# Kernel optimization log

Hardware: AMD Instinct MI355X
Metric: run time of the kernel (lower is better)

The kernel has to match this reference:

```python
import jax, jax.numpy as jnp
import numpy as np

B, N, D_IN, D_OUT = 16, 4096, 256, 128


def setup_inputs() -> dict:
    key = jax.random.key(0)
    ks = jax.random.split(key, 7)
    s_proj = float(np.sqrt(2.0 / D_IN))   # kaiming-ish scale
    s_mlp = float(np.sqrt(2.0 / D_OUT))
    return {
        "X": jax.random.normal(ks[0], (B, N, D_IN), dtype=jnp.float32),
        "W_proj": jax.random.normal(ks[1], (D_IN, D_OUT), dtype=jnp.float32) * s_proj,
        "b_proj": jnp.zeros((D_OUT,), dtype=jnp.float32),
        "W1": jax.random.normal(ks[2], (D_OUT, D_OUT), dtype=jnp.float32) * s_mlp,
        "b1": jnp.zeros((D_OUT,), dtype=jnp.float32),
        "W2": jax.random.normal(ks[3], (D_OUT, D_OUT), dtype=jnp.float32) * s_mlp,
        "b2": jnp.zeros((D_OUT,), dtype=jnp.float32),
    }


def reference(X, W_proj, b_proj, W1, b1, W2, b2):
    # proj: Linear(input_dim, output_dim)
    X = jnp.einsum("bnd,de->bne", X, W_proj) + b_proj
    # mlp: FeedForwardNetwork(D,D,D, num_layers=2) == Linear -> ReLU -> Linear
    X = jax.nn.relu(jnp.einsum("bnd,de->bne", X, W1) + b1)
    X = jnp.einsum("bnd,de->bne", X, W2) + b2
    # leave-one-out sum over the N axis: for each row i, sum of all rows j != i.
    # Identical math to the masked (B,N,N,D) expand-reduce in the torch source.
    return X.sum(axis=1, keepdims=True) - X
```

## Files before the change

kernel.cpp:

```cpp
#include <hip/hip_runtime.h>
#include <stdint.h>

#define D_IN  256
#define D_OUT 128
#define NSEQ  4096
#define NB    16
#define TILE_M 64
#define GRID_M ((NB * NSEQ) / TILE_M)
#define LDS_BYTES 32768

typedef __bf16 bf16x8 __attribute__((ext_vector_type(8)));
typedef float  f32x4  __attribute__((ext_vector_type(4)));

__device__ __forceinline__ unsigned short f2bf(float f) {
  __bf16 h = (__bf16)f;
  union { __bf16 h; unsigned short u; } c; c.h = h;
  return c.u;
}
__device__ __forceinline__ float bf2f(unsigned short u) {
  union { unsigned int u; float f; } a; a.u = ((unsigned int)u) << 16;
  return a.f;
}

__global__ __launch_bounds__(256) void prep(
    const float* __restrict__ Wp, const float* __restrict__ W1, const float* __restrict__ W2,
    const float* __restrict__ bp, const float* __restrict__ b1,
    unsigned short* __restrict__ WaT, unsigned short* __restrict__ W2T, float* __restrict__ be1) {
  int b = blockIdx.x;
  if (b < 128) {
    __shared__ float wp[256];
    int k0 = b * 2;
    wp[threadIdx.x] = Wp[k0 * 128 + threadIdx.x];
    __syncthreads();
    int kk = threadIdx.x >> 7, n = threadIdx.x & 127;
    float s = 0.f;
#pragma unroll 16
    for (int j = 0; j < 128; ++j) s += wp[kk * 128 + j] * W1[j * 128 + n];
    WaT[n * 256 + (k0 + kk)] = f2bf(s);
  } else if (b < 192) {
    int t = (b - 128) * 256 + threadIdx.x;
    int k = t >> 7, n = t & 127;
    W2T[n * 128 + k] = f2bf(W2[t]);
  } else {
    if (threadIdx.x < 128) {
      int n = threadIdx.x;
      float s = b1[n];
#pragma unroll 16
      for (int j = 0; j < 128; ++j) s += bp[j] * W1[j * 128 + n];
      be1[n] = s;
    }
  }
}

template <bool USE_WS>
__global__ __launch_bounds__(256, 3) void fused2(
    const float* __restrict__ X,
    const unsigned short* __restrict__ WaT,
    const unsigned short* __restrict__ W2T,
    const float* __restrict__ be1, const float* __restrict__ b2v,
    unsigned short* __restrict__ Y3, float* __restrict__ out, float* __restrict__ P) {
  extern __shared__ unsigned short smem[];
  unsigned short* bufA = smem;
  unsigned short* bufB = smem + 8192;

  const int tid  = threadIdx.x;
  const int lane = tid & 63;
  const int w    = tid >> 6;
  const int q    = lane >> 4;
  const int l16  = lane & 15;
  const int rowbase = blockIdx.x * TILE_M;
  const int col0 = w * 32 + l16;
  const int col1 = col0 + 16;

  f32x4 acc[4][2];
  bf16x8 bA[4][2], bB[4][2];

#pragma unroll
  for (int ks = 0; ks < 4; ++ks) {
    bA[ks][0] = *(const bf16x8*)(WaT + (size_t)col0 * 256 + ks * 32 + q * 8);
    bA[ks][1] = *(const bf16x8*)(WaT + (size_t)col1 * 256 + ks * 32 + q * 8);
  }

#pragma unroll
  for (int it = 0; it < 8; ++it) {
    int i = tid + it * 256;
    int r = i >> 5, c4 = (i & 31) << 2;
    const float4 v = *(const float4*)(X + (size_t)(rowbase + r) * D_IN + c4);
    ushort4 u; u.x = f2bf(v.x); u.y = f2bf(v.y); u.z = f2bf(v.z); u.w = f2bf(v.w);
    *(ushort4*)(bufA + r * 128 + ((((c4 >> 3) ^ (r & 15)) << 3) + (c4 & 7))) = u;
  }

#pragma unroll
  for (int rt = 0; rt < 4; ++rt) {
    acc[rt][0] = (f32x4){0.f, 0.f, 0.f, 0.f};
    acc[rt][1] = (f32x4){0.f, 0.f, 0.f, 0.f};
  }
  __syncthreads();

  float4 xv[8];
#pragma unroll
  for (int it = 0; it < 8; ++it) {
    int i = tid + it * 256;
    int r = i >> 5, c4 = (i & 31) << 2;
    xv[it] = *(const float4*)(X + (size_t)(rowbase + r) * D_IN + 128 + c4);
  }
#pragma unroll
  for (int ks = 0; ks < 4; ++ks) {
    bB[ks][0] = *(const bf16x8*)(WaT + (size_t)col0 * 256 + 128 + ks * 32 + q * 8);
    bB[ks][1] = *(const bf16x8*)(WaT + (size_t)col1 * 256 + 128 + ks * 32 + q * 8);
  }

#pragma unroll
  for (int ks = 0; ks < 4; ++ks)
#pragma unroll
    for (int rt = 0; rt < 4; ++rt) {
      bf16x8 a = *(const bf16x8*)(bufA + (rt * 16 + l16) * 128 + (((4 * ks + q) ^ l16) << 3));
      acc[rt][0] = __builtin_amdgcn_mfma_f32_16x16x32_bf16(a, bA[ks][0], acc[rt][0], 0, 0, 0);
      acc[rt][1] = __builtin_amdgcn_mfma_f32_16x16x32_bf16(a, bA[ks][1], acc[rt][1], 0, 0, 0);
    }

#pragma unroll
  for (int it = 0; it < 8; ++it) {
    int i = tid + it * 256;
    int r = i >> 5, c4 = (i & 31) << 2;
    ushort4 u; u.x = f2bf(xv[it].x); u.y = f2bf(xv[it].y); u.z = f2bf(xv[it].z); u.w = f2bf(xv[it].w);
    *(ushort4*)(bufB + r * 128 + ((((c4 >> 3) ^ (r & 15)) << 3) + (c4 & 7))) = u;
  }
  __syncthreads();

#pragma unroll
  for (int ks = 0; ks < 4; ++ks) {
    bA[ks][0] = *(const bf16x8*)(W2T + (size_t)col0 * 128 + ks * 32 + q * 8);
    bA[ks][1] = *(const bf16x8*)(W2T + (size_t)col1 * 128 + ks * 32 + q * 8);
  }

#pragma unroll
  for (int ks = 0; ks < 4; ++ks)
#pragma unroll
    for (int rt = 0; rt < 4; ++rt) {
      bf16x8 a = *(const bf16x8*)(bufB + (rt * 16 + l16) * 128 + (((4 * ks + q) ^ l16) << 3));
      acc[rt][0] = __builtin_amdgcn_mfma_f32_16x16x32_bf16(a, bB[ks][0], acc[rt][0], 0, 0, 0);
      acc[rt][1] = __builtin_amdgcn_mfma_f32_16x16x32_bf16(a, bB[ks][1], acc[rt][1], 0, 0, 0);
    }

  {
    const float e0 = be1[col0], e1 = be1[col1];
#pragma unroll
    for (int rt = 0; rt < 4; ++rt)
#pragma unroll
      for (int r = 0; r < 4; ++r) {
        int row = rt * 16 + q * 4 + r;
        int sw = (row & 15) << 3;
        float v0 = acc[rt][0][r] + e0; v0 = v0 > 0.f ? v0 : 0.f;
        float v1 = acc[rt][1][r] + e1; v1 = v1 > 0.f ? v1 : 0.f;
        bufA[row * 128 + ((((col0 >> 3) << 3) ^ sw) + (col0 & 7))] = f2bf(v0);
        bufA[row * 128 + ((((col1 >> 3) << 3) ^ sw) + (col1 & 7))] = f2bf(v1);
      }
  }
  __syncthreads();

#pragma unroll
  for (int rt = 0; rt < 4; ++rt) {
    acc[rt][0] = (f32x4){0.f, 0.f, 0.f, 0.f};
    acc[rt][1] = (f32x4){0.f, 0.f, 0.f, 0.f};
  }
#pragma unroll
  for (int ks = 0; ks < 4; ++ks)
#pragma unroll
    for (int rt = 0; rt < 4; ++rt) {
      bf16x8 a = *(const bf16x8*)(bufA + (rt * 16 + l16) * 128 + (((4 * ks + q) ^ l16) << 3));
      acc[rt][0] = __builtin_amdgcn_mfma_f32_16x16x32_bf16(a, bA[ks][0], acc[rt][0], 0, 0, 0);
      acc[rt][1] = __builtin_amdgcn_mfma_f32_16x16x32_bf16(a, bA[ks][1], acc[rt][1], 0, 0, 0);
    }

  {
    const float bb0 = b2v[col0], bb1 = b2v[col1];
    float s0 = 0.f, s1 = 0.f;
#pragma unroll
    for (int rt = 0; rt < 4; ++rt)
#pragma unroll
      for (int r = 0; r < 4; ++r) {
        int row = rt * 16 + q * 4 + r;
        int sw = (row & 15) << 3;
        float v0 = acc[rt][0][r] + bb0;
        float v1 = acc[rt][1][r] + bb1;
        s0 += v0; s1 += v1;
        bufB[row * 128 + ((((col0 >> 3) << 3) ^ sw) + (col0 & 7))] = f2bf(v0);
        bufB[row * 128 + ((((col1 >> 3) << 3) ^ sw) + (col1 & 7))] = f2bf(v1);
      }
    s0 += __shfl_down(s0, 16); s0 += __shfl_down(s0, 32);
    s1 += __shfl_down(s1, 16); s1 += __shfl_down(s1, 32);
    if (lane < 16) {
      P[(size_t)blockIdx.x * 128 + col0] = s0;
      P[(size_t)blockIdx.x * 128 + col1] = s1;
    }
  }
  __syncthreads();

  if (USE_WS) {
#pragma unroll
    for (int it = 0; it < 4; ++it) {
      int i = tid + it * 256;
      int r = i >> 4, g = i & 15;
      *(uint4*)(Y3 + (size_t)(rowbase + r) * 128 + g * 8) =
          *(const uint4*)(bufB + r * 128 + ((g ^ (r & 15)) << 3));
    }
  } else {
#pragma unroll
    for (int it = 0; it < 8; ++it) {
      int i = tid + it * 256;
      int r = i >> 5, c4 = (i & 31) << 2;
      ushort4 u = *(const ushort4*)(bufB + r * 128 + ((((c4 >> 3) ^ (r & 15)) << 3) + (c4 & 7)));
      float4 v; v.x = bf2f(u.x); v.y = bf2f(u.y); v.z = bf2f(u.z); v.w = bf2f(u.w);
      *(float4*)(out + (size_t)(rowbase + r) * D_OUT + c4) = v;
    }
  }
}

__global__ __launch_bounds__(256) void reduce_S(const float* __restrict__ P, float* __restrict__ S) {
  __shared__ float tmp[128];
  int b = blockIdx.x;
  int col = threadIdx.x & 127;
  int h = threadIdx.x >> 7;
  float s = 0.f;
#pragma unroll
  for (int i = 0; i < 32; ++i) s += P[(size_t)(b * 64 + h * 32 + i) * 128 + col];
  if (h == 1) tmp[col] = s;
  __syncthreads();
  if (h == 0) S[b * 128 + col] = s + tmp[col];
}

__global__ __launch_bounds__(256) void finalize_ws(
    float* __restrict__ out, const unsigned short* __restrict__ Y3, const float* __restrict__ S) {
  size_t g = (size_t)blockIdx.x * 256 + threadIdx.x;
  size_t base = g * 8;
  int row = (int)(base >> 7);
  int col = (int)(base & 127);
  int b = row >> 12;
  uint4 u = *(const uint4*)(Y3 + base);
  float4 s0 = *(const float4*)(S + (b << 7) + col);
  float4 s1 = *(const float4*)(S + (b << 7) + col + 4);
  union { unsigned int uu; float f; } t;
  float4 o0, o1;
  t.uu = u.x << 16;          o0.x = s0.x - t.f;
  t.uu = u.x & 0xFFFF0000u;  o0.y = s0.y - t.f;
  t.uu = u.y << 16;          o0.z = s0.z - t.f;
  t.uu = u.y & 0xFFFF0000u;  o0.w = s0.w - t.f;
  t.uu = u.z << 16;          o1.x = s1.x - t.f;
  t.uu = u.z & 0xFFFF0000u;  o1.y = s1.y - t.f;
  t.uu = u.w << 16;          o1.z = s1.z - t.f;
  t.uu = u.w & 0xFFFF0000u;  o1.w = s1.w - t.f;
  *(float4*)(out + base) = o0;
  *(float4*)(out + base + 4) = o1;
}

__global__ __launch_bounds__(256) void finalize_ip(float* __restrict__ out, const float* __restrict__ S) {
  size_t g = (size_t)blockIdx.x * 256 + threadIdx.x;
  size_t base = g * 8;
  int row = (int)(base >> 7);
  int col = (int)(base & 127);
  int b = row >> 12;
  float4 s0 = *(const float4*)(S + (b << 7) + col);
  float4 s1 = *(const float4*)(S + (b << 7) + col + 4);
  float4 y0 = *(const float4*)(out + base);
  float4 y1 = *(const float4*)(out + base + 4);
  float4 o0, o1;
  o0.x = s0.x - y0.x; o0.y = s0.y - y0.y; o0.z = s0.z - y0.z; o0.w = s0.w - y0.w;
  o1.x = s1.x - y1.x; o1.y = s1.y - y1.y; o1.z = s1.z - y1.z; o1.w = s1.w - y1.w;
  *(float4*)(out + base) = o0;
  *(float4*)(out + base + 4) = o1;
}

extern "C" void kernel_launch(void* const* d_in, const int* in_sizes, int n_in,
                              void* d_out, int out_size, void* d_ws, size_t ws_size,
                              hipStream_t stream) {
  const float* X  = (const float*)d_in[0];
  const float* Wp = (const float*)d_in[1];
  const float* bp = (const float*)d_in[2];
  const float* W1 = (const float*)d_in[3];
  const float* b1 = (const float*)d_in[4];
  const float* W2 = (const float*)d_in[5];
  const float* b2 = (const float*)d_in[6];
  float* out = (float*)d_out;

  char* ws = (char*)d_ws;
  float* S            = (float*)ws;
  float* be1          = (float*)(ws + 8192);
  unsigned short* WaT = (unsigned short*)(ws + 12288);
  unsigned short* W2T = (unsigned short*)(ws + 12288 + 65536);
  float* P            = (float*)(ws + 12288 + 65536 + 32768);
  unsigned short* Y3  = (unsigned short*)(ws + 12288 + 65536 + 32768 + 524288);

  const size_t need = 12288 + 65536 + 32768 + 524288 + (size_t)NB * NSEQ * D_OUT * 2;
  const bool use_ws = ws_size >= need;

  prep<<<193, 256, 0, stream>>>(Wp, W1, W2, bp, b1, WaT, W2T, be1);

  const int fin_blocks = (NB * NSEQ * D_OUT) / (8 * 256);
  if (use_ws) {
    fused2<true><<<GRID_M, 256, LDS_BYTES, stream>>>(X, WaT, W2T, be1, b2, Y3, out, P);
    reduce_S<<<NB, 256, 0, stream>>>(P, S);
    finalize_ws<<<fin_blocks, 256, 0, stream>>>(out, Y3, S);
  } else {
    fused2<false><<<GRID_M, 256, LDS_BYTES, stream>>>(X, WaT, W2T, be1, b2, Y3, out, P);
    reduce_S<<<NB, 256, 0, stream>>>(P, S);
    finalize_ip<<<fin_blocks, 256, 0, stream>>>(out, S);
  }
}
```

Baseline: 134.0 us.

## Fuse per-batch column reduction into GEMM kernel via last-block atomic counter

Removes the separate reduce_S launch: each block bumps a per-batch atomic counter after writing its partial sums, and the last of the 64 blocks for a batch reduces the partials into S. The counters are zeroed in the prep kernel. X loading is also restructured so all 256 input columns are loaded up front into registers (16 float4 per thread) and written to both LDS halves before the first GEMM, rather than overlapping the second-half load with the first MFMA pass. This saves one kernel launch and gap, at the cost of more register pressure, fences, and lost overlap of the second X load.

```diff
diff --git a/kernel.cpp b/kernel.cpp
--- a/kernel.cpp
+++ b/kernel.cpp
@@ -25,7 +25,8 @@
 __global__ __launch_bounds__(256) void prep(
     const float* __restrict__ Wp, const float* __restrict__ W1, const float* __restrict__ W2,
     const float* __restrict__ bp, const float* __restrict__ b1,
-    unsigned short* __restrict__ WaT, unsigned short* __restrict__ W2T, float* __restrict__ be1) {
+    unsigned short* __restrict__ WaT, unsigned short* __restrict__ W2T,
+    float* __restrict__ be1, int* __restrict__ cnt) {
   int b = blockIdx.x;
   if (b < 128) {
     __shared__ float wp[256];
@@ -49,6 +50,7 @@
       for (int j = 0; j < 128; ++j) s += bp[j] * W1[j * 128 + n];
       be1[n] = s;
     }
+    if (threadIdx.x < NB) cnt[threadIdx.x] = 0;
   }
 }
 
@@ -58,10 +60,13 @@
     const unsigned short* __restrict__ WaT,
     const unsigned short* __restrict__ W2T,
     const float* __restrict__ be1, const float* __restrict__ b2v,
-    unsigned short* __restrict__ Y3, float* __restrict__ out, float* __restrict__ P) {
+    unsigned short* __restrict__ Y3, float* __restrict__ out,
+    float* __restrict__ P, float* __restrict__ S, int* __restrict__ cnt) {
   extern __shared__ unsigned short smem[];
   unsigned short* bufA = smem;
   unsigned short* bufB = smem + 8192;
+  __shared__ float red[128];
+  __shared__ int isLast;
 
   const int tid  = threadIdx.x;
   const int lane = tid & 63;
@@ -69,46 +74,44 @@
   const int q    = lane >> 4;
   const int l16  = lane & 15;
   const int rowbase = blockIdx.x * TILE_M;
+  const int bidx = blockIdx.x >> 6;
   const int col0 = w * 32 + l16;
   const int col1 = col0 + 16;
 
-  f32x4 acc[4][2];
+  float4 xv[16];
+#pragma unroll
+  for (int it = 0; it < 16; ++it) {
+    int i = tid + it * 256;
+    int r = i >> 6, c4 = (i & 63) << 2;
+    xv[it] = *(const float4*)(X + (size_t)(rowbase + r) * D_IN + c4);
+  }
+#pragma unroll
+  for (int it = 0; it < 16; ++it) {
+    int i = tid + it * 256;
+    int r = i >> 6, c4 = (i & 63) << 2;
+    unsigned short* dst = (c4 < 128) ? bufA : bufB;
+    int cc = c4 & 127;
+    ushort4 u; u.x = f2bf(xv[it].x); u.y = f2bf(xv[it].y); u.z = f2bf(xv[it].z); u.w = f2bf(xv[it].w);
+    *(ushort4*)(dst + r * 128 + ((((cc >> 3) ^ (r & 15)) << 3) + (cc & 7))) = u;
+  }
+
   bf16x8 bA[4][2], bB[4][2];
-
 #pragma unroll
   for (int ks = 0; ks < 4; ++ks) {
     bA[ks][0] = *(const bf16x8*)(WaT + (size_t)col0 * 256 + ks * 32 + q * 8);
     bA[ks][1] = *(const bf16x8*)(WaT + (size_t)col1 * 256 + ks * 32 + q * 8);
-  }
-
-#pragma unroll
-  for (int it = 0; it < 8; ++it) {
-    int i = tid + it * 256;
-    int r = i >> 5, c4 = (i & 31) << 2;
-    const float4 v = *(const float4*)(X + (size_t)(rowbase + r) * D_IN + c4);
-    ushort4 u; u.x = f2bf(v.x); u.y = f2bf(v.y); u.z = f2bf(v.z); u.w = f2bf(v.w);
-    *(ushort4*)(bufA + r * 128 + ((((c4 >> 3) ^ (r & 15)) << 3) + (c4 & 7))) = u;
-  }
-
+    bB[ks][0] = *(const bf16x8*)(WaT + (size_t)col0 * 256 + 128 + ks * 32 + q * 8);
+    bB[ks][1] = *(const bf16x8*)(WaT + (size_t)col1 * 256 + 128 + ks * 32 + q * 8);
+  }
+  __builtin_amdgcn_sched_barrier(0);
+
+  f32x4 acc[4][2];
 #pragma unroll
   for (int rt = 0; rt < 4; ++rt) {
     acc[rt][0] = (f32x4){0.f, 0.f, 0.f, 0.f};
     acc[rt][1] = (f32x4){0.f, 0.f, 0.f, 0.f};
   }
   __syncthreads();
-
-  float4 xv[8];
-#pragma unroll
-  for (int it = 0; it < 8; ++it) {
-    int i = tid + it * 256;
-    int r = i >> 5, c4 = (i & 31) << 2;
-    xv[it] = *(const float4*)(X + (size_t)(rowbase + r) * D_IN + 128 + c4);
-  }
-#pragma unroll
-  for (int ks = 0; ks < 4; ++ks) {
-    bB[ks][0] = *(const bf16x8*)(WaT + (size_t)col0 * 256 + 128 + ks * 32 + q * 8);
-    bB[ks][1] = *(const bf16x8*)(WaT + (size_t)col1 * 256 + 128 + ks * 32 + q * 8);
-  }
 
 #pragma unroll
   for (int ks = 0; ks < 4; ++ks)
@@ -118,22 +121,6 @@
       acc[rt][0] = __builtin_amdgcn_mfma_f32_16x16x32_bf16(a, bA[ks][0], acc[rt][0], 0, 0, 0);
       acc[rt][1] = __builtin_amdgcn_mfma_f32_16x16x32_bf16(a, bA[ks][1], acc[rt][1], 0, 0, 0);
     }
-
-#pragma unroll
-  for (int it = 0; it < 8; ++it) {
-    int i = tid + it * 256;
-    int r = i >> 5, c4 = (i & 31) << 2;
-    ushort4 u; u.x = f2bf(xv[it].x); u.y = f2bf(xv[it].y); u.z = f2bf(xv[it].z); u.w = f2bf(xv[it].w);
-    *(ushort4*)(bufB + r * 128 + ((((c4 >> 3) ^ (r & 15)) << 3) + (c4 & 7))) = u;
-  }
-  __syncthreads();
-
-#pragma unroll
-  for (int ks = 0; ks < 4; ++ks) {
-    bA[ks][0] = *(const bf16x8*)(W2T + (size_t)col0 * 128 + ks * 32 + q * 8);
-    bA[ks][1] = *(const bf16x8*)(W2T + (size_t)col1 * 128 + ks * 32 + q * 8);
-  }
-
 #pragma unroll
   for (int ks = 0; ks < 4; ++ks)
 #pragma unroll
@@ -142,6 +129,14 @@
       acc[rt][0] = __builtin_amdgcn_mfma_f32_16x16x32_bf16(a, bB[ks][0], acc[rt][0], 0, 0, 0);
       acc[rt][1] = __builtin_amdgcn_mfma_f32_16x16x32_bf16(a, bB[ks][1], acc[rt][1], 0, 0, 0);
     }
+
+#pragma unroll
+  for (int ks = 0; ks < 4; ++ks) {
+    bA[ks][0] = *(const bf16x8*)(W2T + (size_t)col0 * 128 + ks * 32 + q * 8);
+    bA[ks][1] = *(const bf16x8*)(W2T + (size_t)col1 * 128 + ks * 32 + q * 8);
+  }
+  __builtin_amdgcn_sched_barrier(0);
+  __syncthreads();
 
   {
     const float e0 = be1[col0], e1 = be1[col1];
@@ -215,19 +210,25 @@
       *(float4*)(out + (size_t)(rowbase + r) * D_OUT + c4) = v;
     }
   }
-}
-
-__global__ __launch_bounds__(256) void reduce_S(const float* __restrict__ P, float* __restrict__ S) {
-  __shared__ float tmp[128];
-  int b = blockIdx.x;
-  int col = threadIdx.x & 127;
-  int h = threadIdx.x >> 7;
-  float s = 0.f;
-#pragma unroll
-  for (int i = 0; i < 32; ++i) s += P[(size_t)(b * 64 + h * 32 + i) * 128 + col];
-  if (h == 1) tmp[col] = s;
-  __syncthreads();
-  if (h == 0) S[b * 128 + col] = s + tmp[col];
+
+  __threadfence();
+  __syncthreads();
+  if (tid == 0) {
+    int old = atomicAdd(cnt + bidx, 1);
+    isLast = (old == 63);
+  }
+  __syncthreads();
+  if (isLast) {
+    __threadfence();
+    int col = tid & 127, h = tid >> 7;
+    float s = 0.f;
+#pragma unroll
+    for (int i = 0; i < 32; ++i)
+      s += P[(size_t)(bidx * 64 + h * 32 + i) * 128 + col];
+    if (h == 1) red[col] = s;
+    __syncthreads();
+    if (h == 0) S[bidx * 128 + col] = s + red[col];
+  }
 }
 
 __global__ __launch_bounds__(256) void finalize_ws(
@@ -286,6 +287,7 @@
   char* ws = (char*)d_ws;
   float* S            = (float*)ws;
   float* be1          = (float*)(ws + 8192);
+  int*   cnt          = (int*)(ws + 8192 + 2048);
   unsigned short* WaT = (unsigned short*)(ws + 12288);
   unsigned short* W2T = (unsigned short*)(ws + 12288 + 65536);
   float* P            = (float*)(ws + 12288 + 65536 + 32768);
@@ -294,16 +296,14 @@
   const size_t need = 12288 + 65536 + 32768 + 524288 + (size_t)NB * NSEQ * D_OUT * 2;
   const bool use_ws = ws_size >= need;
 
-  prep<<<193, 256, 0, stream>>>(Wp, W1, W2, bp, b1, WaT, W2T, be1);
+  prep<<<193, 256, 0, stream>>>(Wp, W1, W2, bp, b1, WaT, W2T, be1, cnt);
 
   const int fin_blocks = (NB * NSEQ * D_OUT) / (8 * 256);
   if (use_ws) {
-    fused2<true><<<GRID_M, 256, LDS_BYTES, stream>>>(X, WaT, W2T, be1, b2, Y3, out, P);
-    reduce_S<<<NB, 256, 0, stream>>>(P, S);
+    fused2<true><<<GRID_M, 256, LDS_BYTES, stream>>>(X, WaT, W2T, be1, b2, Y3, out, P, S, cnt);
     finalize_ws<<<fin_blocks, 256, 0, stream>>>(out, Y3, S);
   } else {
-    fused2<false><<<GRID_M, 256, LDS_BYTES, stream>>>(X, WaT, W2T, be1, b2, Y3, out, P);
-    reduce_S<<<NB, 256, 0, stream>>>(P, S);
+    fused2<false><<<GRID_M, 256, LDS_BYTES, stream>>>(X, WaT, W2T, be1, b2, Y3, out, P, S, cnt);
     finalize_ip<<<fin_blocks, 256, 0, stream>>>(out, S);
   }
 }
```

Result: slower. 258.6 us (+92.9%).
